# Kernel optimization log

Hardware: AMD Instinct MI355X
Metric: run time of the kernel (lower is better)

The kernel has to match this reference:

```python
import jax, jax.numpy as jnp
import numpy as np

B, TP, TF, C, H, W = 8, 3, 4, 256, 64, 64
BN_EPS = 1e-3  # YOLOX BaseConv BatchNorm2d eps


def setup_inputs() -> dict:
    key = jax.random.key(0)
    ks = jax.random.split(key, 12)
    s = 1.0 / np.sqrt(C)
    return {
        "feature": jax.random.normal(ks[0], (B, TP + 1, C, H, W), jnp.float32),
        "past_time_constant": jax.random.normal(ks[1], (B, TP), jnp.float32),
        "future_time_constant": jax.random.normal(ks[2], (B, TF), jnp.float32),
        # fc_time_constant: Linear(1, C)
        "w_tc": jax.random.normal(ks[3], (C, 1), jnp.float32),
        "b_tc": jax.random.normal(ks[4], (C,), jnp.float32) * 0.1,
        # fc_in: Linear(2C, C)
        "w_in": jax.random.normal(ks[5], (C, 2 * C), jnp.float32) * (1.0 / np.sqrt(2 * C)),
        "b_in": jnp.zeros((C,), jnp.float32),
        # conv_p: 1x1 conv (no bias) + BN + SiLU
        "conv_w": jax.random.normal(ks[6], (C, C), jnp.float32) * s,
        "bn_gamma": jnp.ones((C,), jnp.float32),
        "bn_beta": jnp.zeros((C,), jnp.float32),
        "bn_mean": jax.random.normal(ks[7], (C,), jnp.float32) * 0.1,
        "bn_var": jnp.ones((C,), jnp.float32) + jax.random.uniform(ks[8], (C,)) * 0.1,
        # fc_query / fc_key: Linear(C, C)
        "w_q": jax.random.normal(ks[9], (C, C), jnp.float32) * s,
        "b_q": jnp.zeros((C,), jnp.float32),
        "w_k": jax.random.normal(ks[10], (C, C), jnp.float32) * s,
        "b_k": jnp.zeros((C,), jnp.float32),
        # p_attn: [1,1,C,1,1]
        "p_attn": jnp.ones((1, 1, C, 1, 1), jnp.float32),
    }


def reference(feature, past_time_constant, future_time_constant,
              w_tc, b_tc, w_in, b_in, conv_w, bn_gamma, bn_beta, bn_mean, bn_var,
              w_q, b_q, w_k, b_k, p_attn):
    b, t1, c, h, w = feature.shape
    tp = past_time_constant.shape[1]
    tf = future_time_constant.shape[1]
    silu = jax.nn.silu

    # conv_p = 1x1 conv (bias=False) + BatchNorm(eval) + SiLU, over all TP+1 frames
    x = jnp.einsum('oc,btchw->btohw', conv_w, feature)
    scale = bn_gamma / jnp.sqrt(bn_var + BN_EPS)          # [C]
    x = x * scale[:, None, None] + (bn_beta - bn_mean * scale)[:, None, None]
    feature_p = silu(x)                                    # [B,TP+1,C,H,W]

    # time-constant embeddings: tanh(Linear(1->C))
    ptc = jnp.tanh(past_time_constant[..., None] * w_tc[:, 0] + b_tc)    # [B,TP,C]
    ftc = jnp.tanh(future_time_constant[..., None] * w_tc[:, 0] + b_tc)  # [B,TF,C]

    # past branch: global max+avg pool over HxW, concat, fc_in+SiLU, add ptc
    fp_past = feature_p[:, :-1]                            # [B,TP,C,H,W]
    pool_p = jnp.concatenate([fp_past.max(axis=(-2, -1)), fp_past.mean(axis=(-2, -1))], axis=-1)  # [B,TP,2C]
    attn_in_p = silu(jnp.einsum('oc,btc->bto', w_in, pool_p) + b_in) + ptc  # [B,TP,C]

    # future branch: feature_f = last raw frame broadcast over TF (pool identical per TF)
    last = feature[:, -1]                                  # [B,C,H,W]
    pool_f = jnp.concatenate([last.max(axis=(-2, -1)), last.mean(axis=(-2, -1))], axis=-1)  # [B,2C]
    attn_in_f = silu(pool_f @ w_in.T + b_in)[:, None, :] + ftc  # [B,TF,C]

    q = attn_in_f @ w_q.T + b_q                            # [B,TF,C]
    k = attn_in_p @ w_k.T + b_k                            # [B,TP,C]
    v = (feature_p[:, -1:] - fp_past).reshape(b, tp, c * h * w)  # [B,TP,CHW]

    # NOTE: torch code scales by sqrt(attn_query.size(1)) == sqrt(TF), not sqrt(C)
    attn_w = jnp.einsum('bfc,bpc->bfp', q, k) / jnp.sqrt(jnp.asarray(tf, q.dtype))  # [B,TF,TP]
    attn = jnp.einsum('bfp,bpd->bfd', attn_w, v).reshape(b, tf, c, h, w)

    # residual: feature_f + attn * p_attn / attn_key.size(1) (== TP)
    out = last[:, None] + attn * p_attn / tp               # [B,TF,C,H,W]
    return out
```

## Files before the change

kernel.cpp:

```cpp
#include <hip/hip_runtime.h>

#define B_   8
#define T1_  4
#define TP_  3
#define TF_  4
#define C_   256
#define HW_  4096

#define OFF_FP     0ull
#define OFF_PMAXK  67108864ull
#define OFF_PSUM   67133440ull
#define OFF_RMAX   67158016ull
#define OFF_RSUM   67166208ull
#define OFF_Q      67174400ull
#define OFF_K      67207168ull
#define OFF_AW     67231744ull
#define OFF_WBF    67232128ull
#define OFF_SHIFT  67363200ull

typedef __attribute__((ext_vector_type(8))) short bf16x8;
typedef __attribute__((ext_vector_type(4))) float f32x4;

__device__ __forceinline__ unsigned short f2bf(float f) {
    unsigned int u = __float_as_uint(f);
    u += 0x7fffu + ((u >> 16) & 1u);
    return (unsigned short)(u >> 16);
}
__device__ __forceinline__ unsigned int fkey(float x) {
    unsigned int b = __float_as_uint(x);
    return (b & 0x80000000u) ? ~b : (b | 0x80000000u);
}
__device__ __forceinline__ float funkey(unsigned int k) {
    unsigned int b = (k & 0x80000000u) ? (k ^ 0x80000000u) : ~k;
    return __uint_as_float(b);
}
__device__ __forceinline__ float silu_f(float x) { return x / (1.0f + __expf(-x)); }

__device__ __forceinline__ void dec8(uint4 u, float* f) {
    f[0] = __uint_as_float(u.x << 16); f[1] = __uint_as_float(u.x & 0xffff0000u);
    f[2] = __uint_as_float(u.y << 16); f[3] = __uint_as_float(u.y & 0xffff0000u);
    f[4] = __uint_as_float(u.z << 16); f[5] = __uint_as_float(u.z & 0xffff0000u);
    f[6] = __uint_as_float(u.w << 16); f[7] = __uint_as_float(u.w & 0xffff0000u);
}

__global__ __launch_bounds__(256) void kprep(const float* __restrict__ Wc,
                                             const float* __restrict__ gamma,
                                             const float* __restrict__ beta,
                                             const float* __restrict__ mean,
                                             const float* __restrict__ var,
                                             unsigned short* __restrict__ Wbf,
                                             float* __restrict__ shift) {
    const int tid = threadIdx.x;
    const int idx = blockIdx.x * 1024 + tid * 4;
    const int o = idx >> 8;
    const float sc = gamma[o] * rsqrtf(var[o] + 1e-3f);
    float4 v = *(const float4*)(Wc + idx);
    ushort4 u;
    u.x = f2bf(v.x * sc); u.y = f2bf(v.y * sc);
    u.z = f2bf(v.z * sc); u.w = f2bf(v.w * sc);
    *(ushort4*)(Wbf + idx) = u;
    if (blockIdx.x == 0) {
        float s2 = gamma[tid] * rsqrtf(var[tid] + 1e-3f);
        shift[tid] = beta[tid] - mean[tid] * s2;
    }
}

__global__ __launch_bounds__(256) void k0_rawpool(const float* __restrict__ feature,
                                                  float* __restrict__ rmax,
                                                  float* __restrict__ rsum) {
    const int blk = blockIdx.x;
    const int b = blk >> 8, c = blk & 255;
    const float* base = feature + ((size_t)(b * 4 + 3) * C_ + c) * HW_;
    const int tid = threadIdx.x;
    float mx = -3.4e38f, sm = 0.0f;
    #pragma unroll
    for (int k = 0; k < 4; ++k) {
        float4 v = *(const float4*)(base + (k * 256 + tid) * 4);
        mx = fmaxf(mx, fmaxf(fmaxf(v.x, v.y), fmaxf(v.z, v.w)));
        sm += (v.x + v.y) + (v.z + v.w);
    }
    #pragma unroll
    for (int m = 1; m < 64; m <<= 1) {
        mx = fmaxf(mx, __shfl_xor(mx, m));
        sm += __shfl_xor(sm, m);
    }
    __shared__ float wmx[4], wsm[4];
    const int wave = tid >> 6;
    if ((tid & 63) == 0) { wmx[wave] = mx; wsm[wave] = sm; }
    __syncthreads();
    if (tid == 0) {
        rmax[b * C_ + c] = fmaxf(fmaxf(wmx[0], wmx[1]), fmaxf(wmx[2], wmx[3]));
        rsum[b * C_ + c] = (wsm[0] + wsm[1]) + (wsm[2] + wsm[3]);
    }
}

__global__ __launch_bounds__(256) void k1_conv(
    const float* __restrict__ feature, const unsigned short* __restrict__ Wbf,
    const float* __restrict__ shift,
    unsigned short* __restrict__ fp_out,
    unsigned int* __restrict__ pmaxk, float* __restrict__ psum) {
    __shared__ __align__(16) unsigned short lds_b[2][64 * 40];
    __shared__ float s_shift[256];

    const int tid   = threadIdx.x;
    const int bt    = blockIdx.x >> 6;
    const int hwblk = blockIdx.x & 63;
    const int b = bt >> 2, t = bt & 3;
    const int hw0 = hwblk * 64;
    const int lane = tid & 63;
    const int wave = tid >> 6;
    const int q = lane >> 4;
    const int col = lane & 15;
    const int kg  = wave;
    const int hwl = lane;

    s_shift[tid] = shift[tid];

    const float* Fb = feature + (size_t)bt * C_ * HW_;
    f32x4 acc[4][4] = {};

    float fv[8];
    #pragma unroll
    for (int j = 0; j < 8; ++j)
        fv[j] = Fb[(size_t)(kg * 8 + j) * HW_ + hw0 + hwl];

    for (int it = 0; it < 8; ++it) {
        const int k0 = it * 32;
        uint4 pk;
        pk.x = ((unsigned)f2bf(fv[1]) << 16) | f2bf(fv[0]);
        pk.y = ((unsigned)f2bf(fv[3]) << 16) | f2bf(fv[2]);
        pk.z = ((unsigned)f2bf(fv[5]) << 16) | f2bf(fv[4]);
        pk.w = ((unsigned)f2bf(fv[7]) << 16) | f2bf(fv[6]);
        *(uint4*)&lds_b[it & 1][hwl * 40 + kg * 8] = pk;
        if (it < 7) {
            #pragma unroll
            for (int j = 0; j < 8; ++j)
                fv[j] = Fb[(size_t)(k0 + 32 + kg * 8 + j) * HW_ + hw0 + hwl];
        }
        __syncthreads();
        bf16x8 afr[4], bfr[4];
        #pragma unroll
        for (int mi = 0; mi < 4; ++mi)
            afr[mi] = *(const bf16x8*)(Wbf + (size_t)(wave * 64 + mi * 16 + col) * 256 + k0 + q * 8);
        #pragma unroll
        for (int ni = 0; ni < 4; ++ni)
            bfr[ni] = *(const bf16x8*)&lds_b[it & 1][(ni * 16 + col) * 40 + q * 8];
        #pragma unroll
        for (int mi = 0; mi < 4; ++mi)
            #pragma unroll
            for (int ni = 0; ni < 4; ++ni)
                acc[mi][ni] = __builtin_amdgcn_mfma_f32_16x16x32_bf16(afr[mi], bfr[ni], acc[mi][ni], 0, 0, 0);
    }

    unsigned short* fpo = fp_out + (size_t)bt * C_ * HW_;
    float pmx_r[16], psm_r[16];
    #pragma unroll
    for (int mi = 0; mi < 4; ++mi) {
        #pragma unroll
        for (int r = 0; r < 4; ++r) {
            const int o = wave * 64 + mi * 16 + q * 4 + r;
            const float sh = s_shift[o];
            float mx = -3.4e38f, sm = 0.0f;
            #pragma unroll
            for (int ni = 0; ni < 4; ++ni) {
                float x = acc[mi][ni][r] + sh;
                float s = silu_f(x);
                fpo[(size_t)o * HW_ + hw0 + ni * 16 + col] = f2bf(s);
                mx = fmaxf(mx, s);
                sm += s;
            }
            pmx_r[mi * 4 + r] = mx;
            psm_r[mi * 4 + r] = sm;
        }
    }
    if (t < 3) {
        #pragma unroll
        for (int i = 0; i < 16; ++i) {
            float m = pmx_r[i], s = psm_r[i];
            #pragma unroll
            for (int d = 1; d < 16; d <<= 1) {
                m = fmaxf(m, __shfl_xor(m, d));
                s += __shfl_xor(s, d);
            }
            pmx_r[i] = m; psm_r[i] = s;
        }
        if (col == 0) {
            #pragma unroll
            for (int mi = 0; mi < 4; ++mi)
                #pragma unroll
                for (int r = 0; r < 4; ++r) {
                    const int o = wave * 64 + mi * 16 + q * 4 + r;
                    atomicMax(&pmaxk[(b * 3 + t) * C_ + o], fkey(pmx_r[mi * 4 + r]));
                    atomicAdd(&psum[(b * 3 + t) * C_ + o], psm_r[mi * 4 + r]);
                }
        }
    }
}

__global__ __launch_bounds__(256) void k2_vec(
    const float* __restrict__ past_tc, const float* __restrict__ fut_tc,
    const float* __restrict__ w_tc, const float* __restrict__ b_tc,
    const float* __restrict__ w_in, const float* __restrict__ b_in,
    const float* __restrict__ w_q, const float* __restrict__ b_q,
    const float* __restrict__ w_k, const float* __restrict__ b_k,
    const unsigned int* __restrict__ pmaxk, const float* __restrict__ psum,
    const float* __restrict__ rmax, const float* __restrict__ rsum,
    float* __restrict__ qout, float* __restrict__ kout) {
    __shared__ float pool[512];
    __shared__ float avec[256];
    const int b = blockIdx.x / 7;
    const int idx = blockIdx.x % 7;
    const int o = threadIdx.x;
    const bool pside = (idx < 3);
    if (pside) {
        pool[o]       = funkey(pmaxk[(b * 3 + idx) * C_ + o]);
        pool[256 + o] = psum[(b * 3 + idx) * C_ + o] * (1.0f / 4096.0f);
    } else {
        pool[o]       = rmax[b * C_ + o];
        pool[256 + o] = rsum[b * C_ + o] * (1.0f / 4096.0f);
    }
    __syncthreads();
    float s = b_in[o];
    const float* wr = w_in + (size_t)o * 512;
    #pragma unroll 8
    for (int c = 0; c < 512; ++c) s += wr[c] * pool[c];
    float v = silu_f(s);
    float tcin = pside ? past_tc[b * 3 + idx] : fut_tc[b * 4 + (idx - 3)];
    float tc = tanhf(tcin * w_tc[o] + b_tc[o]);
    avec[o] = v + tc;
    __syncthreads();
    if (pside) {
        float s2 = b_k[o];
        const float* wk = w_k + (size_t)o * 256;
        #pragma unroll 8
        for (int c = 0; c < 256; ++c) s2 += wk[c] * avec[c];
        kout[(b * 3 + idx) * C_ + o] = s2;
    } else {
        float s2 = b_q[o];
        const float* wq = w_q + (size_t)o * 256;
        #pragma unroll 8
        for (int c = 0; c < 256; ++c) s2 += wq[c] * avec[c];
        qout[(b * 4 + (idx - 3)) * C_ + o] = s2;
    }
}

__global__ __launch_bounds__(64) void k2_attnw(const float* __restrict__ qv,
                                               const float* __restrict__ kv,
                                               float* __restrict__ aw) {
    const int i = blockIdx.x;
    const int b = i / 12, rr = i % 12, f = rr / 3, p = rr % 3;
    const int lane = threadIdx.x;
    const float* qp = qv + (b * 4 + f) * C_;
    const float* kp = kv + (b * 3 + p) * C_;
    float s = 0.0f;
    #pragma unroll
    for (int j = 0; j < 4; ++j) s += qp[lane + 64 * j] * kp[lane + 64 * j];
    #pragma unroll
    for (int m = 1; m < 64; m <<= 1) s += __shfl_xor(s, m);
    if (lane == 0) aw[b * 12 + rr] = s * 0.5f;
}

__global__ __launch_bounds__(256) void k3_out(
    const float* __restrict__ feature, const unsigned short* __restrict__ fp,
    const float* __restrict__ aw, const float* __restrict__ p_attn,
    float* __restrict__ out) {
    const int idx = blockIdx.x;
    const int b = idx >> 9;
    const int c = (idx >> 1) & 255;
    const int half = idx & 1;
    const int hw = half * 2048 + threadIdx.x * 8;

    float a[12];
    #pragma unroll
    for (int i = 0; i < 12; ++i) a[i] = aw[b * 12 + i];
    const float pa = p_attn[c] * (1.0f / 3.0f);

    const size_t ts = (size_t)C_ * HW_;
    const size_t base = ((size_t)(b * 4) * C_ + c) * HW_ + hw;

    uint4 u0 = *(const uint4*)(fp + base);
    uint4 u1 = *(const uint4*)(fp + base + ts);
    uint4 u2 = *(const uint4*)(fp + base + 2 * ts);
    uint4 u3 = *(const uint4*)(fp + base + 3 * ts);
    float4 l0 = *(const float4*)(feature + base + 3 * ts);
    float4 l1 = *(const float4*)(feature + base + 3 * ts + 4);

    float f0[8], f1[8], f2[8], f3[8];
    dec8(u0, f0); dec8(u1, f1); dec8(u2, f2); dec8(u3, f3);
    float lastv[8] = {l0.x, l0.y, l0.z, l0.w, l1.x, l1.y, l1.z, l1.w};

    float ov[4][8];
    #pragma unroll
    for (int e = 0; e < 8; ++e) {
        float d0 = f3[e] - f0[e];
        float d1 = f3[e] - f1[e];
        float d2 = f3[e] - f2[e];
        #pragma unroll
        for (int f = 0; f < 4; ++f) {
            float at = a[f * 3 + 0] * d0 + a[f * 3 + 1] * d1 + a[f * 3 + 2] * d2;
            ov[f][e] = lastv[e] + at * pa;
        }
    }
    #pragma unroll
    for (int f = 0; f < 4; ++f) {
        size_t ob = ((size_t)(b * 4 + f) * C_ + c) * HW_ + hw;
        *(float4*)(out + ob)     = make_float4(ov[f][0], ov[f][1], ov[f][2], ov[f][3]);
        *(float4*)(out + ob + 4) = make_float4(ov[f][4], ov[f][5], ov[f][6], ov[f][7]);
    }
}

extern "C" void kernel_launch(void* const* d_in, const int* in_sizes, int n_in,
                              void* d_out, int out_size, void* d_ws, size_t ws_size,
                              hipStream_t stream) {
    const float* feature = (const float*)d_in[0];
    const float* past_tc = (const float*)d_in[1];
    const float* fut_tc  = (const float*)d_in[2];
    const float* w_tc    = (const float*)d_in[3];
    const float* b_tc    = (const float*)d_in[4];
    const float* w_in    = (const float*)d_in[5];
    const float* b_in    = (const float*)d_in[6];
    const float* conv_w  = (const float*)d_in[7];
    const float* gamma   = (const float*)d_in[8];
    const float* beta    = (const float*)d_in[9];
    const float* mean    = (const float*)d_in[10];
    const float* var     = (const float*)d_in[11];
    const float* w_q     = (const float*)d_in[12];
    const float* b_q     = (const float*)d_in[13];
    const float* w_k     = (const float*)d_in[14];
    const float* b_k     = (const float*)d_in[15];
    const float* p_attn  = (const float*)d_in[16];

    char* ws = (char*)d_ws;
    unsigned short* fp  = (unsigned short*)(ws + OFF_FP);
    unsigned int* pmaxk = (unsigned int*)(ws + OFF_PMAXK);
    float* psum = (float*)(ws + OFF_PSUM);
    float* rmax = (float*)(ws + OFF_RMAX);
    float* rsum = (float*)(ws + OFF_RSUM);
    float* qout = (float*)(ws + OFF_Q);
    float* kout = (float*)(ws + OFF_K);
    float* aw   = (float*)(ws + OFF_AW);
    unsigned short* Wbf = (unsigned short*)(ws + OFF_WBF);
    float* shift = (float*)(ws + OFF_SHIFT);

    hipMemsetAsync(ws + OFF_PMAXK, 0, 49152, stream);

    kprep<<<64, 256, 0, stream>>>(conv_w, gamma, beta, mean, var, Wbf, shift);
    k0_rawpool<<<B_ * C_, 256, 0, stream>>>(feature, rmax, rsum);
    k1_conv<<<B_ * T1_ * 64, 256, 0, stream>>>(feature, Wbf, shift, fp, pmaxk, psum);
    k2_vec<<<B_ * 7, 256, 0, stream>>>(past_tc, fut_tc, w_tc, b_tc, w_in, b_in,
                                       w_q, b_q, w_k, b_k, pmaxk, psum, rmax, rsum,
                                       qout, kout);
    k2_attnw<<<B_ * TF_ * TP_, 64, 0, stream>>>(qout, kout, aw);
    k3_out<<<B_ * C_ * 2, 256, 0, stream>>>(feature, fp, aw, p_attn, (float*)d_out);
}
```

Measured before the change: 370.7 us.

## Fuse raw-frame pooling into conv, preload full K tile, merge q/k/attn-weight kernels

Drops the separate raw-pool kernel that re-read the last frame; the conv kernel now computes per-channel max and sum of the raw last frame with wave shuffles and atomics while it loads it. The conv now stages all 256 input channels into LDS up front, using one barrier instead of one per step, and double-buffers the weight fragments from global memory. The q/k projection and attention-weight kernels merge into one 8-block kernel, removing two launches and the intermediate buffers. This trades a much larger LDS footprint (lower occupancy) and many extra shuffles and atomics on the t==3 blocks for less memory traffic and fewer launches. The small fused kernel runs on only 8 blocks.

```diff
diff --git a/kernel.cpp b/kernel.cpp
--- a/kernel.cpp
+++ b/kernel.cpp
@@ -10,10 +10,8 @@
 #define OFF_FP     0ull
 #define OFF_PMAXK  67108864ull
 #define OFF_PSUM   67133440ull
-#define OFF_RMAX   67158016ull
+#define OFF_RMAXK  67158016ull
 #define OFF_RSUM   67166208ull
-#define OFF_Q      67174400ull
-#define OFF_K      67207168ull
 #define OFF_AW     67231744ull
 #define OFF_WBF    67232128ull
 #define OFF_SHIFT  67363200ull
@@ -65,41 +63,13 @@
     }
 }
 
-__global__ __launch_bounds__(256) void k0_rawpool(const float* __restrict__ feature,
-                                                  float* __restrict__ rmax,
-                                                  float* __restrict__ rsum) {
-    const int blk = blockIdx.x;
-    const int b = blk >> 8, c = blk & 255;
-    const float* base = feature + ((size_t)(b * 4 + 3) * C_ + c) * HW_;
-    const int tid = threadIdx.x;
-    float mx = -3.4e38f, sm = 0.0f;
-    #pragma unroll
-    for (int k = 0; k < 4; ++k) {
-        float4 v = *(const float4*)(base + (k * 256 + tid) * 4);
-        mx = fmaxf(mx, fmaxf(fmaxf(v.x, v.y), fmaxf(v.z, v.w)));
-        sm += (v.x + v.y) + (v.z + v.w);
-    }
-    #pragma unroll
-    for (int m = 1; m < 64; m <<= 1) {
-        mx = fmaxf(mx, __shfl_xor(mx, m));
-        sm += __shfl_xor(sm, m);
-    }
-    __shared__ float wmx[4], wsm[4];
-    const int wave = tid >> 6;
-    if ((tid & 63) == 0) { wmx[wave] = mx; wsm[wave] = sm; }
-    __syncthreads();
-    if (tid == 0) {
-        rmax[b * C_ + c] = fmaxf(fmaxf(wmx[0], wmx[1]), fmaxf(wmx[2], wmx[3]));
-        rsum[b * C_ + c] = (wsm[0] + wsm[1]) + (wsm[2] + wsm[3]);
-    }
-}
-
 __global__ __launch_bounds__(256) void k1_conv(
     const float* __restrict__ feature, const unsigned short* __restrict__ Wbf,
     const float* __restrict__ shift,
     unsigned short* __restrict__ fp_out,
-    unsigned int* __restrict__ pmaxk, float* __restrict__ psum) {
-    __shared__ __align__(16) unsigned short lds_b[2][64 * 40];
+    unsigned int* __restrict__ pmaxk, float* __restrict__ psum,
+    unsigned int* __restrict__ rmaxk, float* __restrict__ rsum) {
+    __shared__ __align__(16) unsigned short lds_b[64 * 264];
     __shared__ float s_shift[256];
 
     const int tid   = threadIdx.x;
@@ -111,45 +81,64 @@
     const int wave = tid >> 6;
     const int q = lane >> 4;
     const int col = lane & 15;
-    const int kg  = wave;
-    const int hwl = lane;
 
     s_shift[tid] = shift[tid];
-
     const float* Fb = feature + (size_t)bt * C_ * HW_;
-    f32x4 acc[4][4] = {};
-
-    float fv[8];
-    #pragma unroll
-    for (int j = 0; j < 8; ++j)
-        fv[j] = Fb[(size_t)(kg * 8 + j) * HW_ + hw0 + hwl];
-
-    for (int it = 0; it < 8; ++it) {
-        const int k0 = it * 32;
+
+    #pragma unroll
+    for (int s = 0; s < 8; ++s) {
+        const int cb = s * 32 + wave * 8;
+        float fv[8];
+        #pragma unroll
+        for (int j = 0; j < 8; ++j)
+            fv[j] = Fb[(size_t)(cb + j) * HW_ + hw0 + lane];
+        if (t == 3) {
+            #pragma unroll
+            for (int j = 0; j < 8; ++j) {
+                float mx = fv[j], sm = fv[j];
+                #pragma unroll
+                for (int d = 1; d < 64; d <<= 1) {
+                    mx = fmaxf(mx, __shfl_xor(mx, d));
+                    sm += __shfl_xor(sm, d);
+                }
+                if (lane == 0) {
+                    atomicMax(&rmaxk[b * C_ + cb + j], fkey(mx));
+                    atomicAdd(&rsum[b * C_ + cb + j], sm);
+                }
+            }
+        }
         uint4 pk;
         pk.x = ((unsigned)f2bf(fv[1]) << 16) | f2bf(fv[0]);
         pk.y = ((unsigned)f2bf(fv[3]) << 16) | f2bf(fv[2]);
         pk.z = ((unsigned)f2bf(fv[5]) << 16) | f2bf(fv[4]);
         pk.w = ((unsigned)f2bf(fv[7]) << 16) | f2bf(fv[6]);
-        *(uint4*)&lds_b[it & 1][hwl * 40 + kg * 8] = pk;
+        *(uint4*)&lds_b[lane * 264 + cb] = pk;
+    }
+    __syncthreads();
+
+    f32x4 acc[4][4] = {};
+    bf16x8 afr[2][4];
+    #pragma unroll
+    for (int mi = 0; mi < 4; ++mi)
+        afr[0][mi] = *(const bf16x8*)(Wbf + (size_t)(wave * 64 + mi * 16 + col) * 256 + q * 8);
+    #pragma unroll
+    for (int it = 0; it < 8; ++it) {
+        const int cur = it & 1;
         if (it < 7) {
             #pragma unroll
-            for (int j = 0; j < 8; ++j)
-                fv[j] = Fb[(size_t)(k0 + 32 + kg * 8 + j) * HW_ + hw0 + hwl];
-        }
-        __syncthreads();
-        bf16x8 afr[4], bfr[4];
+            for (int mi = 0; mi < 4; ++mi)
+                afr[cur ^ 1][mi] = *(const bf16x8*)(Wbf + (size_t)(wave * 64 + mi * 16 + col) * 256
+                                                    + (it + 1) * 32 + q * 8);
+        }
+        bf16x8 bfr[4];
+        #pragma unroll
+        for (int ni = 0; ni < 4; ++ni)
+            bfr[ni] = *(const bf16x8*)&lds_b[(ni * 16 + col) * 264 + it * 32 + q * 8];
         #pragma unroll
         for (int mi = 0; mi < 4; ++mi)
-            afr[mi] = *(const bf16x8*)(Wbf + (size_t)(wave * 64 + mi * 16 + col) * 256 + k0 + q * 8);
-        #pragma unroll
-        for (int ni = 0; ni < 4; ++ni)
-            bfr[ni] = *(const bf16x8*)&lds_b[it & 1][(ni * 16 + col) * 40 + q * 8];
-        #pragma unroll
-        for (int mi = 0; mi < 4; ++mi)
             #pragma unroll
             for (int ni = 0; ni < 4; ++ni)
-                acc[mi][ni] = __builtin_amdgcn_mfma_f32_16x16x32_bf16(afr[mi], bfr[ni], acc[mi][ni], 0, 0, 0);
+                acc[mi][ni] = __builtin_amdgcn_mfma_f32_16x16x32_bf16(afr[cur][mi], bfr[ni], acc[mi][ni], 0, 0, 0);
     }
 
     unsigned short* fpo = fp_out + (size_t)bt * C_ * HW_;
@@ -197,67 +186,70 @@
     }
 }
 
-__global__ __launch_bounds__(256) void k2_vec(
+__global__ __launch_bounds__(448) void k2_fused(
     const float* __restrict__ past_tc, const float* __restrict__ fut_tc,
     const float* __restrict__ w_tc, const float* __restrict__ b_tc,
     const float* __restrict__ w_in, const float* __restrict__ b_in,
     const float* __restrict__ w_q, const float* __restrict__ b_q,
     const float* __restrict__ w_k, const float* __restrict__ b_k,
     const unsigned int* __restrict__ pmaxk, const float* __restrict__ psum,
-    const float* __restrict__ rmax, const float* __restrict__ rsum,
-    float* __restrict__ qout, float* __restrict__ kout) {
-    __shared__ float pool[512];
-    __shared__ float avec[256];
-    const int b = blockIdx.x / 7;
-    const int idx = blockIdx.x % 7;
-    const int o = threadIdx.x;
-    const bool pside = (idx < 3);
-    if (pside) {
-        pool[o]       = funkey(pmaxk[(b * 3 + idx) * C_ + o]);
-        pool[256 + o] = psum[(b * 3 + idx) * C_ + o] * (1.0f / 4096.0f);
-    } else {
-        pool[o]       = rmax[b * C_ + o];
-        pool[256 + o] = rsum[b * C_ + o] * (1.0f / 4096.0f);
+    const unsigned int* __restrict__ rmaxk, const float* __restrict__ rsum,
+    float* __restrict__ aw) {
+    __shared__ float s_pool[7][512];
+    __shared__ float s_avec[7][256];
+    __shared__ float s_qk[7][256];
+    const int b = blockIdx.x;
+    const int w = threadIdx.x >> 6;
+    const int lane = threadIdx.x & 63;
+    const bool pside = (w < 3);
+
+    #pragma unroll
+    for (int e = 0; e < 8; ++e) {
+        int c = lane * 8 + e;
+        float v;
+        if (c < 256) {
+            v = pside ? funkey(pmaxk[(b * 3 + w) * C_ + c]) : funkey(rmaxk[b * C_ + c]);
+        } else {
+            int cc = c - 256;
+            v = (pside ? psum[(b * 3 + w) * C_ + cc] : rsum[b * C_ + cc]) * (1.0f / 4096.0f);
+        }
+        s_pool[w][c] = v;
     }
     __syncthreads();
-    float s = b_in[o];
-    const float* wr = w_in + (size_t)o * 512;
-    #pragma unroll 8
-    for (int c = 0; c < 512; ++c) s += wr[c] * pool[c];
-    float v = silu_f(s);
-    float tcin = pside ? past_tc[b * 3 + idx] : fut_tc[b * 4 + (idx - 3)];
-    float tc = tanhf(tcin * w_tc[o] + b_tc[o]);
-    avec[o] = v + tc;
+    const float tcin = pside ? past_tc[b * 3 + w] : fut_tc[b * 4 + (w - 3)];
+    #pragma unroll
+    for (int i = 0; i < 4; ++i) {
+        const int o = i * 64 + lane;
+        float s = b_in[o];
+        const float* wr = w_in + (size_t)o * 512;
+        #pragma unroll 8
+        for (int c = 0; c < 512; ++c) s += wr[c] * s_pool[w][c];
+        float tc = tanhf(tcin * w_tc[o] + b_tc[o]);
+        s_avec[w][o] = silu_f(s) + tc;
+    }
     __syncthreads();
-    if (pside) {
-        float s2 = b_k[o];
-        const float* wk = w_k + (size_t)o * 256;
+    #pragma unroll
+    for (int i = 0; i < 4; ++i) {
+        const int o = i * 64 + lane;
+        const float* wm = (pside ? w_k : w_q) + (size_t)o * 256;
+        float s = pside ? b_k[o] : b_q[o];
         #pragma unroll 8
-        for (int c = 0; c < 256; ++c) s2 += wk[c] * avec[c];
-        kout[(b * 3 + idx) * C_ + o] = s2;
-    } else {
-        float s2 = b_q[o];
-        const float* wq = w_q + (size_t)o * 256;
-        #pragma unroll 8
-        for (int c = 0; c < 256; ++c) s2 += wq[c] * avec[c];
-        qout[(b * 4 + (idx - 3)) * C_ + o] = s2;
-    }
-}
-
-__global__ __launch_bounds__(64) void k2_attnw(const float* __restrict__ qv,
-                                               const float* __restrict__ kv,
-                                               float* __restrict__ aw) {
-    const int i = blockIdx.x;
-    const int b = i / 12, rr = i % 12, f = rr / 3, p = rr % 3;
-    const int lane = threadIdx.x;
-    const float* qp = qv + (b * 4 + f) * C_;
-    const float* kp = kv + (b * 3 + p) * C_;
-    float s = 0.0f;
-    #pragma unroll
-    for (int j = 0; j < 4; ++j) s += qp[lane + 64 * j] * kp[lane + 64 * j];
-    #pragma unroll
-    for (int m = 1; m < 64; m <<= 1) s += __shfl_xor(s, m);
-    if (lane == 0) aw[b * 12 + rr] = s * 0.5f;
+        for (int c = 0; c < 256; ++c) s += wm[c] * s_avec[w][c];
+        s_qk[w][o] = s;
+    }
+    __syncthreads();
+    if (w < 4) {
+        #pragma unroll
+        for (int p = 0; p < 3; ++p) {
+            float part = 0.0f;
+            #pragma unroll
+            for (int j = 0; j < 4; ++j)
+                part += s_qk[3 + w][lane + 64 * j] * s_qk[p][lane + 64 * j];
+            #pragma unroll
+            for (int d = 1; d < 64; d <<= 1) part += __shfl_xor(part, d);
+            if (lane == 0) aw[b * 12 + w * 3 + p] = part * 0.5f;
+        }
+    }
 }
 
 __global__ __launch_bounds__(256) void k3_out(
@@ -334,22 +326,18 @@
     unsigned short* fp  = (unsigned short*)(ws + OFF_FP);
     unsigned int* pmaxk = (unsigned int*)(ws + OFF_PMAXK);
     float* psum = (float*)(ws + OFF_PSUM);
-    float* rmax = (float*)(ws + OFF_RMAX);
+    unsigned int* rmaxk = (unsigned int*)(ws + OFF_RMAXK);
     float* rsum = (float*)(ws + OFF_RSUM);
-    float* qout = (float*)(ws + OFF_Q);
-    float* kout = (float*)(ws + OFF_K);
     float* aw   = (float*)(ws + OFF_AW);
     unsigned short* Wbf = (unsigned short*)(ws + OFF_WBF);
     float* shift = (float*)(ws + OFF_SHIFT);
 
-    hipMemsetAsync(ws + OFF_PMAXK, 0, 49152, stream);
+    hipMemsetAsync(ws + OFF_PMAXK, 0, 65536, stream);
 
     kprep<<<64, 256, 0, stream>>>(conv_w, gamma, beta, mean, var, Wbf, shift);
-    k0_rawpool<<<B_ * C_, 256, 0, stream>>>(feature, rmax, rsum);
-    k1_conv<<<B_ * T1_ * 64, 256, 0, stream>>>(feature, Wbf, shift, fp, pmaxk, psum);
-    k2_vec<<<B_ * 7, 256, 0, stream>>>(past_tc, fut_tc, w_tc, b_tc, w_in, b_in,
-                                       w_q, b_q, w_k, b_k, pmaxk, psum, rmax, rsum,
-                                       qout, kout);
-    k2_attnw<<<B_ * TF_ * TP_, 64, 0, stream>>>(qout, kout, aw);
+    k1_conv<<<B_ * T1_ * 64, 256, 0, stream>>>(feature, Wbf, shift, fp,
+                                               pmaxk, psum, rmaxk, rsum);
+    k2_fused<<<B_, 448, 0, stream>>>(past_tc, fut_tc, w_tc, b_tc, w_in, b_in,
+                                     w_q, b_q, w_k, b_k, pmaxk, psum, rmaxk, rsum, aw);
     k3_out<<<B_ * C_ * 2, 256, 0, stream>>>(feature, fp, aw, p_attn, (float*)d_out);
 }
```

New measurement: 556.8 us. +50.2%, slower.
